# Performance work log

Measured on AMD Instinct MI355X. Metric: run time of the kernel, lower is better.

Reference implementation:

```python
import jax, jax.numpy as jnp
import numpy as np

MARGIN = 2.0   # self.m
SCALE = 30.0   # cosine-head logit scale


def setup_inputs() -> dict:
    key = jax.random.key(0)
    k1, k2, k3 = jax.random.split(key, 3)
    B, D, C = 8192, 256, 5994
    emb = jax.random.normal(k1, (B, D), dtype=jnp.float32)
    W = jax.random.normal(k2, (C, D), dtype=jnp.float32) * 0.05
    y = jax.random.randint(k3, (B,), 0, C, dtype=jnp.int32)
    # first half domain 0 (main), second half domain 1 (target)
    y_d = jnp.concatenate([jnp.zeros(B // 2, jnp.int32), jnp.ones(B // 2, jnp.int32)])
    return {"emb": emb, "W": W, "y": y, "y_d": y_d}


def _clf_head(emb, W, y):
    # cosine-similarity classifier + cross-entropy (standard ASV clf head)
    e = emb / (jnp.linalg.norm(emb, axis=1, keepdims=True) + 1e-12)
    w = W / (jnp.linalg.norm(W, axis=1, keepdims=True) + 1e-12)
    logits = SCALE * (e @ w.T)                     # [B, C]
    logp = jax.nn.log_softmax(logits, axis=-1)
    loss = -jnp.mean(jnp.take_along_axis(logp, y[:, None], axis=1))
    acc = jnp.mean((jnp.argmax(logits, axis=-1) == y).astype(jnp.float32))
    return loss, acc


def reference(emb, W, y, y_d):
    B, D = emb.shape
    H = B // 2
    idx = jnp.arange(B)
    # faithful scatter: domain-0 rows -> main_emb[i]; domain-1 rows -> target_emb[i % H]
    # out-of-range sentinel H is dropped (rows with wrong domain stay zero)
    main_idx = jnp.where(y_d == 0, idx, H)
    tgt_idx = jnp.where(y_d != 0, idx % H, H)
    main_emb = jnp.zeros((H, D), emb.dtype).at[main_idx].set(emb, mode="drop")
    target_emb = jnp.zeros((H, D), emb.dtype).at[tgt_idx].set(emb, mode="drop")

    loss_c, acc = _clf_head(emb, W, y)

    # pairwise diffs: even rows main[i]-main[(i+1)%H] (label 1), odd rows main[i]-target[i] (label 0)
    pos_diff = main_emb - jnp.roll(main_emb, -1, axis=0)  # [H, D]
    neg_diff = main_emb - target_emb                      # [H, D]
    das_diff = jnp.stack([pos_diff, neg_diff], axis=1).reshape(B, D)
    das_label = jnp.tile(jnp.array([1.0, 0.0], emb.dtype), H)  # [B]

    das_dist = jnp.linalg.norm(das_diff, axis=1)
    das_loss = jnp.mean((1.0 - das_label) * das_dist ** 2
                        + das_label * jnp.maximum(MARGIN - das_dist, 0.0) ** 2)
    das_dist_mean = jnp.mean(jax.lax.stop_gradient(das_dist))
    return (loss_c, das_loss, acc, das_dist_mean)
```

## Files before the change

### kernel.cpp

```cpp
#include <hip/hip_runtime.h>
#include <hip/hip_bf16.h>

#define B_ROWS 8192
#define DIM 256
#define C_CLS 5994
#define N_CHUNK 188
#define NSPL 8
#define H_HALF 4096
#define SCALE_F 30.0f
#define MAXL 30.0f
#define EXPC 43.2808512266689f

typedef _Float16 half8 __attribute__((ext_vector_type(8)));
typedef float f32x16 __attribute__((ext_vector_type(16)));
typedef unsigned long long u64;

__global__ __launch_bounds__(256)
void k_pack(const float* __restrict__ emb, const float* __restrict__ W,
            _Float16* __restrict__ en_blk, _Float16* __restrict__ wn_blk,
            float* __restrict__ rne, float* __restrict__ rnw) {
  __shared__ float ssm[256];
  __shared__ float rnl[32];
  const int b = blockIdx.x;
  const bool isW = b >= (B_ROWS/32);
  const int tile = isW ? b - (B_ROWS/32) : b;
  const int t = threadIdx.x;
  const int l31 = t & 31;
  const int row = tile*32 + l31;
  const float* __restrict__ src = isW ? W : emb;
  const bool rv = (!isW) || (row < C_CLS);

  float v[4][8];
  float ss = 0.f;
  #pragma unroll
  for (int i=0;i<4;i++) {
    const int d0 = ((t>>6) + i*4)*16 + ((t>>5)&1)*8;
    if (rv) {
      float4 x0 = *(const float4*)(src + (size_t)row*DIM + d0);
      float4 x1 = *(const float4*)(src + (size_t)row*DIM + d0 + 4);
      v[i][0]=x0.x; v[i][1]=x0.y; v[i][2]=x0.z; v[i][3]=x0.w;
      v[i][4]=x1.x; v[i][5]=x1.y; v[i][6]=x1.z; v[i][7]=x1.w;
      ss += x0.x*x0.x + x0.y*x0.y + x0.z*x0.z + x0.w*x0.w
          + x1.x*x1.x + x1.y*x1.y + x1.z*x1.z + x1.w*x1.w;
    } else {
      #pragma unroll
      for (int j=0;j<8;j++) v[i][j] = 0.f;
    }
  }
  ssm[t] = ss;
  __syncthreads();
  if (t < 32) {
    float s = 0.f;
    #pragma unroll
    for (int j=0;j<8;j++) s += ssm[t + j*32];
    float rn = 1.0f/(sqrtf(s) + 1e-12f);
    rnl[t] = rn;
    int rw = tile*32 + t;
    if (!isW) rne[rw] = rn;
    else if (rw < C_CLS) rnw[rw] = rn;
  }
  __syncthreads();
  const float rn = rnl[l31];
  _Float16* __restrict__ dst = (isW ? wn_blk : en_blk) + (size_t)tile*8192;
  #pragma unroll
  for (int i=0;i<4;i++) {
    half8 h;
    #pragma unroll
    for (int j=0;j<8;j++) h[j] = (_Float16)(v[i][j]*rn);
    *(half8*)(dst + t*8 + i*2048) = h;
  }
}

__global__ __launch_bounds__(256, 2)
void k_logits(const _Float16* __restrict__ en_blk, const _Float16* __restrict__ wn_blk,
              float* __restrict__ psum, u64* __restrict__ pkey) {
  const int split = blockIdx.x & (NSPL-1);
  const int panel = blockIdx.x / NSPL;
  const int wid  = threadIdx.x >> 6;
  const int lane = threadIdx.x & 63;
  const int l31  = lane & 31;
  const int lh   = lane >> 5;
  const int tile = panel*4 + wid;

  half8 a[16];
  const _Float16* ab = en_blk + (size_t)tile*8192 + lane*8;
  #pragma unroll
  for (int k=0;k<16;k++) a[k] = *(const half8*)(ab + k*512);

  float ssum[16], vmax[16]; unsigned cmax[16];
  #pragma unroll
  for (int r=0;r<16;r++){ ssum[r]=0.f; vmax[r]=-2.f; cmax[r]=0u; }

  const _Float16* wb = wn_blk + lane*8;
  half8 b0[8], b1[8];
  {
    const _Float16* p = wb + (size_t)split*8192;
    #pragma unroll
    for (int k=0;k<8;k++) b0[k] = *(const half8*)(p + k*512);
    #pragma unroll
    for (int k=0;k<8;k++) b1[k] = *(const half8*)(p + (k+8)*512);
  }

  for (int c = split; c < N_CHUNK; c += NSPL) {
    const int cn = c + NSPL;
    const _Float16* p = wb + (size_t)cn*8192;
    f32x16 acc = {};
    #pragma unroll
    for (int k=0;k<8;k++)
      acc = __builtin_amdgcn_mfma_f32_32x32x16_f16(a[k], b0[k], acc, 0,0,0);
    if (cn < N_CHUNK) {
      #pragma unroll
      for (int k=0;k<8;k++) b0[k] = *(const half8*)(p + k*512);
    }
    #pragma unroll
    for (int k=0;k<8;k++)
      acc = __builtin_amdgcn_mfma_f32_32x32x16_f16(a[k+8], b1[k], acc, 0,0,0);
    if (cn < N_CHUNK) {
      #pragma unroll
      for (int k=0;k<8;k++) b1[k] = *(const half8*)(p + (k+8)*512);
    }
    const unsigned colu = (unsigned)(c*32 + l31);
    #pragma unroll
    for (int r=0;r<16;r++) {
      float x = acc[r];
      ssum[r] += exp2f(fmaf(x, EXPC, -EXPC));
      if (x > vmax[r]) { vmax[r] = x; cmax[r] = colu; }
    }
  }

  u64 key[16];
  #pragma unroll
  for (int r=0;r<16;r++)
    key[r] = ((u64)__float_as_uint(vmax[r] + 2.0f) << 32) | (unsigned)(~cmax[r]);
  #pragma unroll
  for (int off=1; off<32; off<<=1) {
    #pragma unroll
    for (int r=0;r<16;r++) {
      ssum[r] += __shfl_xor(ssum[r], off);
      u64 o = __shfl_xor(key[r], off);
      key[r] = o > key[r] ? o : key[r];
    }
  }
  if (l31 == 0) {
    const int rowbase = tile*32;
    #pragma unroll
    for (int r=0;r<16;r++) {
      int row = rowbase + (r&3) + 8*(r>>2) + 4*lh;
      psum[split*B_ROWS + row] = ssum[r];
      pkey[split*B_ROWS + row] = key[r];
    }
  }
}

__global__ __launch_bounds__(256)
void k_tail(const float* __restrict__ emb, const float* __restrict__ W,
            const int* __restrict__ y, const int* __restrict__ y_d,
            const float* __restrict__ rne, const float* __restrict__ rnw,
            const float* __restrict__ psum, const u64* __restrict__ pkey,
            float* __restrict__ accum) {
  __shared__ float s0[4], s1[4];
  const int wid = threadIdx.x >> 6, lane = threadIdx.x & 63;
  if (blockIdx.x < 128) {
    float lacc = 0.f, cacc = 0.f;
    for (int row = blockIdx.x*4 + wid; row < B_ROWS; row += 512) {
      const int yc = y[row];
      float4 e = *(const float4*)(emb + (size_t)row*DIM + lane*4);
      float4 w = *(const float4*)(W + (size_t)yc*DIM + lane*4);
      float d = e.x*w.x + e.y*w.y + e.z*w.z + e.w*w.w;
      #pragma unroll
      for (int off=1; off<64; off<<=1) d += __shfl_xor(d, off);
      float S = 0.f; u64 km = 0;
      if (lane < NSPL) {
        S = psum[lane*B_ROWS + row];
        km = pkey[lane*B_ROWS + row];
      }
      #pragma unroll
      for (int off=1; off<NSPL; off<<=1) {
        S += __shfl_xor(S, off);
        u64 o = __shfl_xor(km, off);
        if (o > km) km = o;
      }
      if (lane == 0) {
        float ly = SCALE_F * d * rne[row] * rnw[yc];
        lacc += MAXL + logf(S) - ly;
        unsigned col = ~(unsigned)km;
        cacc += (col == (unsigned)yc) ? 1.f : 0.f;
      }
    }
    if (lane == 0) { s0[wid] = lacc; s1[wid] = cacc; }
    __syncthreads();
    if (threadIdx.x == 0) {
      atomicAdd(&accum[0], s0[0]+s0[1]+s0[2]+s0[3]);
      atomicAdd(&accum[1], s1[0]+s1[1]+s1[2]+s1[3]);
    }
  } else {
    float a2 = 0.f, a3 = 0.f;
    for (int i = (blockIdx.x-128)*4 + wid; i < H_HALF; i += 256) {
      const int j = (i+1) & (H_HALF-1);
      const int di = y_d[i], dj = y_d[j], dih = y_d[i + H_HALF];
      float4 z = {0.f,0.f,0.f,0.f};
      float4 mi = (di==0)  ? *(const float4*)(emb + (size_t)i*DIM + lane*4) : z;
      float4 mj = (dj==0)  ? *(const float4*)(emb + (size_t)j*DIM + lane*4) : z;
      float4 ti = (dih!=0) ? *(const float4*)(emb + (size_t)(i+H_HALF)*DIM + lane*4)
                           : ((di!=0) ? *(const float4*)(emb + (size_t)i*DIM + lane*4) : z);
      float px = mi.x-mj.x, py = mi.y-mj.y, pz = mi.z-mj.z, pw = mi.w-mj.w;
      float nx = mi.x-ti.x, ny = mi.y-ti.y, nz = mi.z-ti.z, nw = mi.w-ti.w;
      float sp = px*px+py*py+pz*pz+pw*pw;
      float sn = nx*nx+ny*ny+nz*nz+nw*nw;
      #pragma unroll
      for (int off=1; off<64; off<<=1) { sp += __shfl_xor(sp, off); sn += __shfl_xor(sn, off); }
      if (lane == 0) {
        float dp = sqrtf(sp), dn = sqrtf(sn);
        float m = fmaxf(2.0f - dp, 0.f);
        a2 += m*m + dn*dn;
        a3 += dp + dn;
      }
    }
    if (lane == 0) { s0[wid] = a2; s1[wid] = a3; }
    __syncthreads();
    if (threadIdx.x == 0) {
      atomicAdd(&accum[2], s0[0]+s0[1]+s0[2]+s0[3]);
      atomicAdd(&accum[3], s1[0]+s1[1]+s1[2]+s1[3]);
    }
  }
}

__global__ void k_fin(const float* __restrict__ accum, float* __restrict__ out) {
  if (threadIdx.x == 0) {
    out[0] = accum[0] * (1.0f/B_ROWS);
    out[1] = accum[2] * (1.0f/B_ROWS);
    out[2] = accum[1] * (1.0f/B_ROWS);
    out[3] = accum[3] * (1.0f/B_ROWS);
  }
}

extern "C" void kernel_launch(void* const* d_in, const int* in_sizes, int n_in,
                              void* d_out, int out_size, void* d_ws, size_t ws_size,
                              hipStream_t stream) {
  const float* emb = (const float*)d_in[0];
  const float* W   = (const float*)d_in[1];
  const int*   y   = (const int*)d_in[2];
  const int*   y_d = (const int*)d_in[3];

  char* ws = (char*)d_ws;
  const size_t EN_OFF   = 0;
  const size_t WN_OFF   = EN_OFF  + (size_t)256*16384;
  const size_t RNE_OFF  = WN_OFF  + (size_t)N_CHUNK*16384;
  const size_t RNW_OFF  = RNE_OFF + (size_t)B_ROWS*4;
  const size_t PSUM_OFF = RNW_OFF + 24064;
  const size_t PKEY_OFF = PSUM_OFF + (size_t)NSPL*B_ROWS*4;
  const size_t ACC_OFF  = PKEY_OFF + (size_t)NSPL*B_ROWS*8;

  _Float16* en_blk = (_Float16*)(ws + EN_OFF);
  _Float16* wn_blk = (_Float16*)(ws + WN_OFF);
  float*    rne   = (float*)(ws + RNE_OFF);
  float*    rnw   = (float*)(ws + RNW_OFF);
  float*    psum  = (float*)(ws + PSUM_OFF);
  u64*      pkey  = (u64*)(ws + PKEY_OFF);
  float*    accum = (float*)(ws + ACC_OFF);

  hipMemsetAsync(accum, 0, 4*sizeof(float), stream);

  k_pack<<<B_ROWS/32 + N_CHUNK, 256, 0, stream>>>(emb, W, en_blk, wn_blk, rne, rnw);
  k_logits<<<64*NSPL, 256, 0, stream>>>(en_blk, wn_blk, psum, pkey);
  k_tail<<<192, 256, 0, stream>>>(emb, W, y, y_d, rne, rnw, psum, pkey, accum);
  k_fin<<<1, 64, 0, stream>>>(accum, (float*)d_out);
}
```

Before: 83.03 us.

## Pack argmax into 32-bit keys, use native exp2, fold memset and finalize into kernels

The argmax tracking in the logits kernel becomes a single 32-bit key: the truncated value bits with the column index in the low 13 bits. This replaces the 64-bit compare/select and shuffles and halves pkey traffic. exp2f is swapped for the hardware exp2 builtin, and the main loop is peeled so the last iteration has no conditional prefetch. The accumulator memset moves into k_pack, and k_fin is replaced by a last-block-done atomic counter in k_tail, removing two launches. Truncating value bits can change argmax ties or near-ties, which risks small accuracy differences.

After: 76.37 us. 8.0% less time.

```diff
diff --git a/kernel.cpp b/kernel.cpp
--- a/kernel.cpp
+++ b/kernel.cpp
@@ -11,20 +11,30 @@
 #define MAXL 30.0f
 #define EXPC 43.2808512266689f
 
+#if defined(__has_builtin)
+#if __has_builtin(__builtin_amdgcn_exp2f)
+#define EXP2(x) __builtin_amdgcn_exp2f(x)
+#endif
+#endif
+#ifndef EXP2
+#define EXP2(x) exp2f(x)
+#endif
+
 typedef _Float16 half8 __attribute__((ext_vector_type(8)));
 typedef float f32x16 __attribute__((ext_vector_type(16)));
-typedef unsigned long long u64;
 
 __global__ __launch_bounds__(256)
 void k_pack(const float* __restrict__ emb, const float* __restrict__ W,
             _Float16* __restrict__ en_blk, _Float16* __restrict__ wn_blk,
-            float* __restrict__ rne, float* __restrict__ rnw) {
+            float* __restrict__ rne, float* __restrict__ rnw,
+            float* __restrict__ accum) {
   __shared__ float ssm[256];
   __shared__ float rnl[32];
   const int b = blockIdx.x;
+  const int t = threadIdx.x;
+  if (b == 0 && t < 8) accum[t] = 0.f;
   const bool isW = b >= (B_ROWS/32);
   const int tile = isW ? b - (B_ROWS/32) : b;
-  const int t = threadIdx.x;
   const int l31 = t & 31;
   const int row = tile*32 + l31;
   const float* __restrict__ src = isW ? W : emb;
@@ -73,7 +83,7 @@
 
 __global__ __launch_bounds__(256, 2)
 void k_logits(const _Float16* __restrict__ en_blk, const _Float16* __restrict__ wn_blk,
-              float* __restrict__ psum, u64* __restrict__ pkey) {
+              float* __restrict__ psum, unsigned* __restrict__ pkey) {
   const int split = blockIdx.x & (NSPL-1);
   const int panel = blockIdx.x / NSPL;
   const int wid  = threadIdx.x >> 6;
@@ -87,57 +97,67 @@
   #pragma unroll
   for (int k=0;k<16;k++) a[k] = *(const half8*)(ab + k*512);
 
-  float ssum[16], vmax[16]; unsigned cmax[16];
-  #pragma unroll
-  for (int r=0;r<16;r++){ ssum[r]=0.f; vmax[r]=-2.f; cmax[r]=0u; }
-
-  const _Float16* wb = wn_blk + lane*8;
+  float ssum[16]; unsigned key[16];
+  #pragma unroll
+  for (int r=0;r<16;r++){ ssum[r]=0.f; key[r]=0u; }
+
+  const int nit = (N_CHUNK - split + NSPL - 1) / NSPL;
+  const _Float16* p = wn_blk + (size_t)split*8192 + lane*8;
+  const ptrdiff_t STEP = (ptrdiff_t)NSPL*8192;
+
   half8 b0[8], b1[8];
+  #pragma unroll
+  for (int k=0;k<8;k++) b0[k] = *(const half8*)(p + k*512);
+  #pragma unroll
+  for (int k=0;k<8;k++) b1[k] = *(const half8*)(p + (k+8)*512);
+
+  unsigned colu = (unsigned)(split*32 + l31);
+  for (int it = 0; it < nit-1; ++it) {
+    const _Float16* pn = p + STEP;
+    f32x16 acc = {};
+    #pragma unroll
+    for (int k=0;k<8;k++)
+      acc = __builtin_amdgcn_mfma_f32_32x32x16_f16(a[k], b0[k], acc, 0,0,0);
+    #pragma unroll
+    for (int k=0;k<8;k++) b0[k] = *(const half8*)(pn + k*512);
+    #pragma unroll
+    for (int k=0;k<8;k++)
+      acc = __builtin_amdgcn_mfma_f32_32x32x16_f16(a[k+8], b1[k], acc, 0,0,0);
+    #pragma unroll
+    for (int k=0;k<8;k++) b1[k] = *(const half8*)(pn + (k+8)*512);
+    #pragma unroll
+    for (int r=0;r<16;r++) {
+      float x = acc[r];
+      ssum[r] += EXP2(fmaf(x, EXPC, -EXPC));
+      unsigned ky = (__float_as_uint(x + 2.0f) & 0xFFFFE000u) | colu;
+      key[r] = ky > key[r] ? ky : key[r];
+    }
+    colu += NSPL*32;
+    p = pn;
+  }
   {
-    const _Float16* p = wb + (size_t)split*8192;
-    #pragma unroll
-    for (int k=0;k<8;k++) b0[k] = *(const half8*)(p + k*512);
-    #pragma unroll
-    for (int k=0;k<8;k++) b1[k] = *(const half8*)(p + (k+8)*512);
-  }
-
-  for (int c = split; c < N_CHUNK; c += NSPL) {
-    const int cn = c + NSPL;
-    const _Float16* p = wb + (size_t)cn*8192;
     f32x16 acc = {};
     #pragma unroll
     for (int k=0;k<8;k++)
       acc = __builtin_amdgcn_mfma_f32_32x32x16_f16(a[k], b0[k], acc, 0,0,0);
-    if (cn < N_CHUNK) {
-      #pragma unroll
-      for (int k=0;k<8;k++) b0[k] = *(const half8*)(p + k*512);
-    }
     #pragma unroll
     for (int k=0;k<8;k++)
       acc = __builtin_amdgcn_mfma_f32_32x32x16_f16(a[k+8], b1[k], acc, 0,0,0);
-    if (cn < N_CHUNK) {
-      #pragma unroll
-      for (int k=0;k<8;k++) b1[k] = *(const half8*)(p + (k+8)*512);
-    }
-    const unsigned colu = (unsigned)(c*32 + l31);
     #pragma unroll
     for (int r=0;r<16;r++) {
       float x = acc[r];
-      ssum[r] += exp2f(fmaf(x, EXPC, -EXPC));
-      if (x > vmax[r]) { vmax[r] = x; cmax[r] = colu; }
-    }
-  }
-
-  u64 key[16];
-  #pragma unroll
-  for (int r=0;r<16;r++)
-    key[r] = ((u64)__float_as_uint(vmax[r] + 2.0f) << 32) | (unsigned)(~cmax[r]);
+      ssum[r] += EXP2(fmaf(x, EXPC, -EXPC));
+      unsigned ky = (__float_as_uint(x + 2.0f) & 0xFFFFE000u) | colu;
+      key[r] = ky > key[r] ? ky : key[r];
+    }
+  }
+
   #pragma unroll
   for (int off=1; off<32; off<<=1) {
     #pragma unroll
     for (int r=0;r<16;r++) {
       ssum[r] += __shfl_xor(ssum[r], off);
-      u64 o = __shfl_xor(key[r], off);
+      unsigned o = __shfl_xor(key[r], off);
       key[r] = o > key[r] ? o : key[r];
     }
   }
@@ -156,8 +176,8 @@
 void k_tail(const float* __restrict__ emb, const float* __restrict__ W,
             const int* __restrict__ y, const int* __restrict__ y_d,
             const float* __restrict__ rne, const float* __restrict__ rnw,
-            const float* __restrict__ psum, const u64* __restrict__ pkey,
-            float* __restrict__ accum) {
+            const float* __restrict__ psum, const unsigned* __restrict__ pkey,
+            float* __restrict__ accum, float* __restrict__ out) {
   __shared__ float s0[4], s1[4];
   const int wid = threadIdx.x >> 6, lane = threadIdx.x & 63;
   if (blockIdx.x < 128) {
@@ -169,7 +189,7 @@
       float d = e.x*w.x + e.y*w.y + e.z*w.z + e.w*w.w;
       #pragma unroll
       for (int off=1; off<64; off<<=1) d += __shfl_xor(d, off);
-      float S = 0.f; u64 km = 0;
+      float S = 0.f; unsigned km = 0u;
       if (lane < NSPL) {
         S = psum[lane*B_ROWS + row];
         km = pkey[lane*B_ROWS + row];
@@ -177,14 +197,13 @@
       #pragma unroll
       for (int off=1; off<NSPL; off<<=1) {
         S += __shfl_xor(S, off);
-        u64 o = __shfl_xor(km, off);
+        unsigned o = __shfl_xor(km, off);
         if (o > km) km = o;
       }
       if (lane == 0) {
         float ly = SCALE_F * d * rne[row] * rnw[yc];
         lacc += MAXL + logf(S) - ly;
-        unsigned col = ~(unsigned)km;
-        cacc += (col == (unsigned)yc) ? 1.f : 0.f;
+        cacc += ((km & 0x1FFFu) == (unsigned)yc) ? 1.f : 0.f;
       }
     }
     if (lane == 0) { s0[wid] = lacc; s1[wid] = cacc; }
@@ -223,14 +242,20 @@
       atomicAdd(&accum[3], s1[0]+s1[1]+s1[2]+s1[3]);
     }
   }
-}
-
-__global__ void k_fin(const float* __restrict__ accum, float* __restrict__ out) {
   if (threadIdx.x == 0) {
-    out[0] = accum[0] * (1.0f/B_ROWS);
-    out[1] = accum[2] * (1.0f/B_ROWS);
-    out[2] = accum[1] * (1.0f/B_ROWS);
-    out[3] = accum[3] * (1.0f/B_ROWS);
+    __threadfence();
+    unsigned* cnt = (unsigned*)(accum + 4);
+    unsigned done = atomicAdd(cnt, 1u);
+    if (done == 191u) {
+      float v0 = atomicAdd(&accum[0], 0.f);
+      float v1 = atomicAdd(&accum[1], 0.f);
+      float v2 = atomicAdd(&accum[2], 0.f);
+      float v3 = atomicAdd(&accum[3], 0.f);
+      out[0] = v0 * (1.0f/B_ROWS);
+      out[1] = v2 * (1.0f/B_ROWS);
+      out[2] = v1 * (1.0f/B_ROWS);
+      out[3] = v3 * (1.0f/B_ROWS);
+    }
   }
 }
 
@@ -249,20 +274,17 @@
   const size_t RNW_OFF  = RNE_OFF + (size_t)B_ROWS*4;
   const size_t PSUM_OFF = RNW_OFF + 24064;
   const size_t PKEY_OFF = PSUM_OFF + (size_t)NSPL*B_ROWS*4;
-  const size_t ACC_OFF  = PKEY_OFF + (size_t)NSPL*B_ROWS*8;
+  const size_t ACC_OFF  = PKEY_OFF + (size_t)NSPL*B_ROWS*4;
 
   _Float16* en_blk = (_Float16*)(ws + EN_OFF);
   _Float16* wn_blk = (_Float16*)(ws + WN_OFF);
   float*    rne   = (float*)(ws + RNE_OFF);
   float*    rnw   = (float*)(ws + RNW_OFF);
   float*    psum  = (float*)(ws + PSUM_OFF);
-  u64*      pkey  = (u64*)(ws + PKEY_OFF);
+  unsigned* pkey  = (unsigned*)(ws + PKEY_OFF);
   float*    accum = (float*)(ws + ACC_OFF);
 
-  hipMemsetAsync(accum, 0, 4*sizeof(float), stream);
-
-  k_pack<<<B_ROWS/32 + N_CHUNK, 256, 0, stream>>>(emb, W, en_blk, wn_blk, rne, rnw);
+  k_pack<<<B_ROWS/32 + N_CHUNK, 256, 0, stream>>>(emb, W, en_blk, wn_blk, rne, rnw, accum);
   k_logits<<<64*NSPL, 256, 0, stream>>>(en_blk, wn_blk, psum, pkey);
-  k_tail<<<192, 256, 0, stream>>>(emb, W, y, y_d, rne, rnw, psum, pkey, accum);
-  k_fin<<<1, 64, 0, stream>>>(accum, (float*)d_out);
-}
+  k_tail<<<192, 256, 0, stream>>>(emb, W, y, y_d, rne, rnw, psum, pkey, accum, (float*)d_out);
+}
```
